# Kernel tuning notes

Hardware: AMD Instinct MI355X
Metric: run time of the kernel (lower is better)

The kernel has to match this reference:

```python
import jax, jax.numpy as jnp
import numpy as np

D_IN = 1024
D_OUT = 1024
NUM_HEADS = 16
HEAD_DIM = D_OUT // NUM_HEADS


def setup_inputs() -> dict:
    key = jax.random.key(0)
    ks = jax.random.split(key, 6)
    s = 0.02
    return {
        "x": jax.random.normal(ks[0], (4, 2048, D_IN), dtype=jnp.float32),
        "Wq": jax.random.normal(ks[1], (D_IN, D_OUT), dtype=jnp.float32) * s,
        "Wk": jax.random.normal(ks[2], (D_IN, D_OUT), dtype=jnp.float32) * s,
        "Wv": jax.random.normal(ks[3], (D_IN, D_OUT), dtype=jnp.float32) * s,
        "Wo": jax.random.normal(ks[4], (D_OUT, D_OUT), dtype=jnp.float32) * s,
        "bo": jax.random.normal(ks[5], (D_OUT,), dtype=jnp.float32) * s,
    }


def reference(x, Wq, Wk, Wv, Wo, bo):
    B, S, _ = x.shape
    # QKV projections (no bias), split into heads: [B, H, S, Dh]
    def split_heads(t):
        return t.reshape(B, S, NUM_HEADS, HEAD_DIM).transpose(0, 2, 1, 3)

    q = split_heads(x @ Wq)
    k = split_heads(x @ Wk)
    v = split_heads(x @ Wv)

    # causal scores [B, H, S, S]; note: original masks BEFORE scaling,
    # but -inf is scale-invariant so softmax(scores/sqrt(d)) with mask is identical.
    scores = jnp.einsum("bhqd,bhkd->bhqk", q, k) / jnp.sqrt(jnp.asarray(HEAD_DIM, x.dtype))
    causal = jnp.tril(jnp.ones((S, S), dtype=bool))
    scores = jnp.where(causal, scores, -jnp.inf)
    attn = jax.nn.softmax(scores, axis=-1)
    # dropout p=0.0 -> identity
    ctx = jnp.einsum("bhqk,bhkd->bhqd", attn, v)  # [B, H, S, Dh]
    ctx = ctx.transpose(0, 2, 1, 3).reshape(B, S, D_OUT)
    return ctx @ Wo + bo
```

## Files before the change

### kernel.cpp

```cpp
#include <hip/hip_runtime.h>
#include <hip/hip_bf16.h>
#include <math.h>


typedef __attribute__((ext_vector_type(8))) short short8;
typedef __attribute__((ext_vector_type(4))) float f32x4;

#define MFMA_BF16(a, b, c) __builtin_amdgcn_mfma_f32_16x16x32_bf16((a), (b), (c), 0, 0, 0)

__device__ __forceinline__ void gld_lds16(const void* g, void* l) {
  __builtin_amdgcn_global_load_lds((const __attribute__((address_space(1))) void*)g,
                                   (__attribute__((address_space(3))) void*)l, 16, 0, 0);
}

__global__ void cast_f32_bf16(const float* __restrict__ in, __hip_bfloat16* __restrict__ out) {
  int i = blockIdx.x * blockDim.x + threadIdx.x;
  float4 v = ((const float4*)in)[i];
  __align__(8) __hip_bfloat16 tmp[4] = {__float2bfloat16(v.x), __float2bfloat16(v.y),
                                        __float2bfloat16(v.z), __float2bfloat16(v.w)};
  ((ushort4*)out)[i] = *(const ushort4*)tmp;
}

__global__ void transpose_cast_w4(const float* __restrict__ W0, const float* __restrict__ W1,
                                  const float* __restrict__ W2, const float* __restrict__ W3,
                                  __hip_bfloat16* __restrict__ T0, __hip_bfloat16* __restrict__ T1,
                                  __hip_bfloat16* __restrict__ T2, __hip_bfloat16* __restrict__ T3) {
  const int z = blockIdx.z;
  const float* W = (z == 0) ? W0 : (z == 1) ? W1 : (z == 2) ? W2 : W3;
  __hip_bfloat16* Wt = (z == 0) ? T0 : (z == 1) ? T1 : (z == 2) ? T2 : T3;
  __shared__ float tile[32][33];
  int tx = threadIdx.x, ty = threadIdx.y;
  int n0 = blockIdx.x * 32, k0 = blockIdx.y * 32;
#pragma unroll
  for (int i = 0; i < 4; ++i)
    tile[ty + i * 8][tx] = W[(size_t)(k0 + ty + i * 8) * 1024 + n0 + tx];
  __syncthreads();
#pragma unroll
  for (int i = 0; i < 4; ++i)
    Wt[(size_t)(n0 + ty + i * 8) * 1024 + k0 + tx] = __float2bfloat16(tile[tx][ty + i * 8]);
}

__global__ __launch_bounds__(256, 2) void gemm_qkv(
    const __hip_bfloat16* __restrict__ A, const __hip_bfloat16* __restrict__ Bt,
    __hip_bfloat16* __restrict__ q, __hip_bfloat16* __restrict__ k,
    __hip_bfloat16* __restrict__ vT) {
  __shared__ __align__(16) __hip_bfloat16 As[128 * 32];
  __shared__ __align__(16) __hip_bfloat16 Bs[128 * 32];
  const int tid = threadIdx.x;
  const int lane = tid & 63, wid = tid >> 6;
  const int quad = lane >> 4, l16 = lane & 15;
  const int part = blockIdx.x >> 3;
  const int n0 = (blockIdx.x & 7) * 128;
  const int gn0 = part * 1024 + n0;
  const int m0 = blockIdx.y * 128;
  const int wm = (wid & 1) * 64, wn = (wid >> 1) * 64;

  f32x4 acc[4][4] = {};

  for (int k0 = 0; k0 < 1024; k0 += 32) {
    __syncthreads();
#pragma unroll
    for (int i = 0; i < 2; ++i) {
      int sbase = __builtin_amdgcn_readfirstlane(wid * 64 + i * 256);
      int s = sbase + lane;
      int row = s >> 2, ch = s & 3;
      gld_lds16(A + (size_t)(m0 + row) * 1024 + k0 + ch * 8, &As[sbase * 8]);
      gld_lds16(Bt + (size_t)(gn0 + row) * 1024 + k0 + ch * 8, &Bs[sbase * 8]);
    }
    __syncthreads();

    short8 af[4], bfr[4];
#pragma unroll
    for (int t = 0; t < 4; ++t) {
      af[t] = *(const short8*)&As[(wm + t * 16 + l16) * 32 + quad * 8];
      bfr[t] = *(const short8*)&Bs[(wn + t * 16 + l16) * 32 + quad * 8];
    }
#pragma unroll
    for (int mt = 0; mt < 4; ++mt)
#pragma unroll
      for (int nt = 0; nt < 4; ++nt)
        acc[mt][nt] = MFMA_BF16(af[mt], bfr[nt], acc[mt][nt]);
  }

  if (part < 2) {
    __hip_bfloat16* C = (part == 0) ? q : k;
#pragma unroll
    for (int mt = 0; mt < 4; ++mt)
#pragma unroll
      for (int nt = 0; nt < 4; ++nt) {
        int row = m0 + wm + mt * 16 + quad * 4;
        int col = n0 + wn + nt * 16 + l16;
#pragma unroll
        for (int r = 0; r < 4; ++r)
          C[(size_t)(row + r) * 1024 + col] = __float2bfloat16(acc[mt][nt][r]);
      }
  } else {
#pragma unroll
    for (int mt = 0; mt < 4; ++mt)
#pragma unroll
      for (int nt = 0; nt < 4; ++nt) {
        int row = m0 + wm + mt * 16 + quad * 4;
        int nn = n0 + wn + nt * 16 + l16;
        __align__(8) __hip_bfloat16 p4[4];
#pragma unroll
        for (int r = 0; r < 4; ++r) p4[r] = __float2bfloat16(acc[mt][nt][r]);
        *(ushort4*)(vT + (size_t)nn * 8192 + row) = *(const ushort4*)p4;
      }
  }
}

__global__ __launch_bounds__(256, 2) void gemm_bt_f32out(
    const __hip_bfloat16* __restrict__ A, const __hip_bfloat16* __restrict__ Bt,
    float* __restrict__ C, const float* __restrict__ bias, int M, int N, int K) {
  __shared__ __align__(16) __hip_bfloat16 As[128 * 32];
  __shared__ __align__(16) __hip_bfloat16 Bs[128 * 32];
  const int tid = threadIdx.x;
  const int lane = tid & 63, wid = tid >> 6;
  const int quad = lane >> 4, l16 = lane & 15;
  const int m0 = blockIdx.y * 128, n0 = blockIdx.x * 128;
  const int wm = (wid & 1) * 64, wn = (wid >> 1) * 64;

  f32x4 acc[4][4] = {};

  for (int k0 = 0; k0 < K; k0 += 32) {
    __syncthreads();
#pragma unroll
    for (int i = 0; i < 2; ++i) {
      int sbase = __builtin_amdgcn_readfirstlane(wid * 64 + i * 256);
      int s = sbase + lane;
      int row = s >> 2, ch = s & 3;
      gld_lds16(A + (size_t)(m0 + row) * K + k0 + ch * 8, &As[sbase * 8]);
      gld_lds16(Bt + (size_t)(n0 + row) * K + k0 + ch * 8, &Bs[sbase * 8]);
    }
    __syncthreads();

    short8 af[4], bfr[4];
#pragma unroll
    for (int t = 0; t < 4; ++t) {
      af[t] = *(const short8*)&As[(wm + t * 16 + l16) * 32 + quad * 8];
      bfr[t] = *(const short8*)&Bs[(wn + t * 16 + l16) * 32 + quad * 8];
    }
#pragma unroll
    for (int mt = 0; mt < 4; ++mt)
#pragma unroll
      for (int nt = 0; nt < 4; ++nt)
        acc[mt][nt] = MFMA_BF16(af[mt], bfr[nt], acc[mt][nt]);
  }

#pragma unroll
  for (int mt = 0; mt < 4; ++mt)
#pragma unroll
    for (int nt = 0; nt < 4; ++nt) {
      int row = m0 + wm + mt * 16 + quad * 4;
      int col = n0 + wn + nt * 16 + l16;
      float b = bias[col];
#pragma unroll
      for (int r = 0; r < 4; ++r)
        C[(size_t)(row + r) * N + col] = acc[mt][nt][r] + b;
    }
}

__global__ __launch_bounds__(256, 2) void attn_kernel(
    const __hip_bfloat16* __restrict__ Q, const __hip_bfloat16* __restrict__ Km,
    const __hip_bfloat16* __restrict__ vT, __hip_bfloat16* __restrict__ ctx) {
  const int bid = blockIdx.x;
  const int p = bid & 7, h = (bid >> 3) & 15, b = bid >> 7;
  const size_t rbase = (size_t)b * 2048;
  const int tid = threadIdx.x, lane = tid & 63, wid = tid >> 6;
  const int quad = lane >> 4, l16 = lane & 15;

  __shared__ __align__(16) __hip_bfloat16 Ks[64 * 72];
  __shared__ __align__(16) __hip_bfloat16 Vs[64 * 72];
  __shared__ __align__(16) __hip_bfloat16 Ps[4][32 * 76];

  const float CSCL = 0.18033688011112042f;
  const float NEG_BIG = -1e30f;

#pragma unroll 1
  for (int sub = 0; sub < 2; ++sub) {
    const int qt = sub ? (15 - p) : p;
    const int q0 = qt * 128;

    short8 qf[2][2];
#pragma unroll
    for (int mt = 0; mt < 2; ++mt)
#pragma unroll
      for (int kc = 0; kc < 2; ++kc)
        qf[mt][kc] = *(const short8*)(Q + (rbase + q0 + wid * 32 + mt * 16 + l16) * 1024 +
                                      h * 64 + kc * 32 + quad * 8);

    f32x4 o[2][4] = {};
    f32x4 lp[2] = {};
    const int wave_max_row = q0 + wid * 32 + 31;
    const int ktiles = q0 / 64 + 2;

#pragma unroll 1
    for (int kt = 0; kt < ktiles; ++kt) {
      const int kbase = kt * 64;
      __syncthreads();
      {
#pragma unroll
        for (int i = 0; i < 2; ++i) {
          int s = tid + i * 256;
          int krow = s >> 3, ch = s & 7;
          *(short8*)&Ks[krow * 72 + ch * 8] =
              *(const short8*)(Km + (rbase + kbase + krow) * 1024 + h * 64 + ch * 8);
        }
      }
      {
#pragma unroll
        for (int i = 0; i < 2; ++i) {
          int s = tid + i * 256;
          int d = s >> 3, ch = s & 7;
          *(short8*)&Vs[d * 72 + ch * 8] =
              *(const short8*)(vT + (size_t)(h * 64 + d) * 8192 + rbase + kbase + ch * 8);
        }
      }
      __syncthreads();

      if (kbase <= wave_max_row) {
        short8 kf[4][2];
#pragma unroll
        for (int nt = 0; nt < 4; ++nt)
#pragma unroll
          for (int kc = 0; kc < 2; ++kc)
            kf[nt][kc] = *(const short8*)&Ks[(nt * 16 + l16) * 72 + kc * 32 + quad * 8];
        f32x4 s[2][4];
#pragma unroll
        for (int mt = 0; mt < 2; ++mt)
#pragma unroll
          for (int nt = 0; nt < 4; ++nt) {
            f32x4 sv = {0.f, 0.f, 0.f, 0.f};
            sv = MFMA_BF16(qf[mt][0], kf[nt][0], sv);
            sv = MFMA_BF16(qf[mt][1], kf[nt][1], sv);
            s[mt][nt] = sv;
          }
        if (kbase + 63 > q0 + wid * 32) {
#pragma unroll
          for (int mt = 0; mt < 2; ++mt)
#pragma unroll
            for (int nt = 0; nt < 4; ++nt)
#pragma unroll
              for (int r = 0; r < 4; ++r) {
                int row = q0 + wid * 32 + mt * 16 + quad * 4 + r;
                int col = kbase + nt * 16 + l16;
                if (col > row) s[mt][nt][r] = NEG_BIG;
              }
        }
#pragma unroll
        for (int mt = 0; mt < 2; ++mt) {
#pragma unroll
          for (int nt = 0; nt < 4; ++nt)
#pragma unroll
            for (int r = 0; r < 4; ++r) {
              float pv = __builtin_amdgcn_exp2f(s[mt][nt][r] * CSCL);
              s[mt][nt][r] = pv;
              lp[mt][r] += pv;
            }
#pragma unroll
          for (int nt = 0; nt < 4; ++nt)
#pragma unroll
            for (int r = 0; r < 4; ++r)
              Ps[wid][(mt * 16 + quad * 4 + r) * 76 + nt * 16 + l16] =
                  __float2bfloat16(s[mt][nt][r]);
        }
        short8 pa[2][2], vf[4][2];
#pragma unroll
        for (int mt = 0; mt < 2; ++mt)
#pragma unroll
          for (int ch = 0; ch < 2; ++ch)
            pa[mt][ch] = *(const short8*)&Ps[wid][(mt * 16 + l16) * 76 + ch * 32 + quad * 8];
#pragma unroll
        for (int dt = 0; dt < 4; ++dt)
#pragma unroll
          for (int ch = 0; ch < 2; ++ch)
            vf[dt][ch] = *(const short8*)&Vs[(dt * 16 + l16) * 72 + ch * 32 + quad * 8];
#pragma unroll
        for (int mt = 0; mt < 2; ++mt)
#pragma unroll
          for (int dt = 0; dt < 4; ++dt) {
            o[mt][dt] = MFMA_BF16(pa[mt][0], vf[dt][0], o[mt][dt]);
            o[mt][dt] = MFMA_BF16(pa[mt][1], vf[dt][1], o[mt][dt]);
          }
      }
    }

#pragma unroll
    for (int mt = 0; mt < 2; ++mt) {
#pragma unroll
      for (int msk = 1; msk <= 8; msk <<= 1)
#pragma unroll
        for (int r = 0; r < 4; ++r)
          lp[mt][r] += __shfl_xor(lp[mt][r], msk, 64);
      float inv[4];
#pragma unroll
      for (int r = 0; r < 4; ++r) inv[r] = 1.f / lp[mt][r];
#pragma unroll
      for (int dt = 0; dt < 4; ++dt)
#pragma unroll
        for (int r = 0; r < 4; ++r)
          ctx[(rbase + q0 + wid * 32 + mt * 16 + quad * 4 + r) * 1024 + h * 64 + dt * 16 + l16] =
              __float2bfloat16(o[mt][dt][r] * inv[r]);
    }
  }
}

extern "C" void kernel_launch(void* const* d_in, const int* in_sizes, int n_in,
                              void* d_out, int out_size, void* d_ws, size_t ws_size,
                              hipStream_t stream) {
  const float* x  = (const float*)d_in[0];
  const float* Wq = (const float*)d_in[1];
  const float* Wk = (const float*)d_in[2];
  const float* Wv = (const float*)d_in[3];
  const float* Wo = (const float*)d_in[4];
  const float* bo = (const float*)d_in[5];
  float* out = (float*)d_out;

  char* ws = (char*)d_ws;
  const size_t MB = 1024ull * 1024ull;
  __hip_bfloat16* q   = (__hip_bfloat16*)(ws);
  __hip_bfloat16* k   = (__hip_bfloat16*)(ws + 16 * MB);
  __hip_bfloat16* vT  = (__hip_bfloat16*)(ws + 32 * MB);
  __hip_bfloat16* woT = (__hip_bfloat16*)(ws + 48 * MB);
  __hip_bfloat16* ctx = q;

  char* outc = (char*)d_out;
  __hip_bfloat16* xb    = (__hip_bfloat16*)(outc);
  __hip_bfloat16* wcatT = (__hip_bfloat16*)(outc + 16 * MB);

  cast_f32_bf16<<<8192, 256, 0, stream>>>(x, xb);
  transpose_cast_w4<<<dim3(32, 32, 4), dim3(32, 8), 0, stream>>>(
      Wq, Wk, Wv, Wo, wcatT, wcatT + 1024 * 1024, wcatT + 2048 * 1024, woT);

  gemm_qkv<<<dim3(24, 64), 256, 0, stream>>>(xb, wcatT, q, k, vT);

  attn_kernel<<<512, 256, 0, stream>>>(q, k, vT, ctx);

  gemm_bt_f32out<<<dim3(8, 64), 256, 0, stream>>>(ctx, woT, out, bo, 8192, 1024, 1024);
}
```

Before: 265.7 us.

## Load K/V fragments directly from global per wave, drop LDS staging and barriers

The attention kernel no longer stages K and V tiles through shared memory with block-wide barriers. Each wave now loads its MFMA fragments straight from global memory and runs only as many key tiles as its own causal extent needs. The softmax scale is folded into the Q projection epilogue, which removes a multiply per score. The cost is that the four waves in a block each re-read K/V from global or L2 instead of sharing one LDS copy, and the loads are not pipelined, so latency may be exposed.

Result: slower. 321.2 us (+20.9%).

```diff
diff --git a/kernel.cpp b/kernel.cpp
--- a/kernel.cpp
+++ b/kernel.cpp
@@ -82,8 +82,10 @@
         acc[mt][nt] = MFMA_BF16(af[mt], bfr[nt], acc[mt][nt]);
   }
 
+  const float CSCL = 0.18033688011112042f;
   if (part < 2) {
     __hip_bfloat16* C = (part == 0) ? q : k;
+    const float scl = (part == 0) ? CSCL : 1.0f;
 #pragma unroll
     for (int mt = 0; mt < 4; ++mt)
 #pragma unroll
@@ -92,7 +94,7 @@
         int col = n0 + wn + nt * 16 + l16;
 #pragma unroll
         for (int r = 0; r < 4; ++r)
-          C[(size_t)(row + r) * 1024 + col] = __float2bfloat16(acc[mt][nt][r]);
+          C[(size_t)(row + r) * 1024 + col] = __float2bfloat16(acc[mt][nt][r] * scl);
       }
   } else {
 #pragma unroll
@@ -169,12 +171,12 @@
   const int tid = threadIdx.x, lane = tid & 63, wid = tid >> 6;
   const int quad = lane >> 4, l16 = lane & 15;
 
-  __shared__ __align__(16) __hip_bfloat16 Ks[64 * 72];
-  __shared__ __align__(16) __hip_bfloat16 Vs[64 * 72];
   __shared__ __align__(16) __hip_bfloat16 Ps[4][32 * 76];
 
-  const float CSCL = 0.18033688011112042f;
   const float NEG_BIG = -1e30f;
+
+  const __hip_bfloat16* Kbase = Km + (rbase + l16) * 1024 + h * 64 + quad * 8;
+  const __hip_bfloat16* Vbase = vT + (size_t)(h * 64 + l16) * 8192 + rbase + quad * 8;
 
 #pragma unroll 1
   for (int sub = 0; sub < 2; ++sub) {
@@ -192,97 +194,77 @@
     f32x4 o[2][4] = {};
     f32x4 lp[2] = {};
     const int wave_max_row = q0 + wid * 32 + 31;
-    const int ktiles = q0 / 64 + 2;
+    const int ktiles_w = (wave_max_row >> 6) + 1;
 
 #pragma unroll 1
-    for (int kt = 0; kt < ktiles; ++kt) {
+    for (int kt = 0; kt < ktiles_w; ++kt) {
       const int kbase = kt * 64;
-      __syncthreads();
-      {
-#pragma unroll
-        for (int i = 0; i < 2; ++i) {
-          int s = tid + i * 256;
-          int krow = s >> 3, ch = s & 7;
-          *(short8*)&Ks[krow * 72 + ch * 8] =
-              *(const short8*)(Km + (rbase + kbase + krow) * 1024 + h * 64 + ch * 8);
+
+      short8 kf[4][2];
+#pragma unroll
+      for (int nt = 0; nt < 4; ++nt)
+#pragma unroll
+        for (int kc = 0; kc < 2; ++kc)
+          kf[nt][kc] = *(const short8*)(Kbase + (size_t)(kbase + nt * 16) * 1024 + kc * 32);
+      short8 vf[4][2];
+#pragma unroll
+      for (int dt = 0; dt < 4; ++dt)
+#pragma unroll
+        for (int ch = 0; ch < 2; ++ch)
+          vf[dt][ch] = *(const short8*)(Vbase + (size_t)dt * 16 * 8192 + kbase + ch * 32);
+
+      f32x4 s[2][4];
+#pragma unroll
+      for (int mt = 0; mt < 2; ++mt)
+#pragma unroll
+        for (int nt = 0; nt < 4; ++nt) {
+          f32x4 sv = {0.f, 0.f, 0.f, 0.f};
+          sv = MFMA_BF16(qf[mt][0], kf[nt][0], sv);
+          sv = MFMA_BF16(qf[mt][1], kf[nt][1], sv);
+          s[mt][nt] = sv;
         }
+      if (kbase + 63 > q0 + wid * 32) {
+#pragma unroll
+        for (int mt = 0; mt < 2; ++mt)
+#pragma unroll
+          for (int nt = 0; nt < 4; ++nt)
+#pragma unroll
+            for (int r = 0; r < 4; ++r) {
+              int row = q0 + wid * 32 + mt * 16 + quad * 4 + r;
+              int col = kbase + nt * 16 + l16;
+              if (col > row) s[mt][nt][r] = NEG_BIG;
+            }
       }
-      {
-#pragma unroll
-        for (int i = 0; i < 2; ++i) {
-          int s = tid + i * 256;
-          int d = s >> 3, ch = s & 7;
-          *(short8*)&Vs[d * 72 + ch * 8] =
-              *(const short8*)(vT + (size_t)(h * 64 + d) * 8192 + rbase + kbase + ch * 8);
+#pragma unroll
+      for (int mt = 0; mt < 2; ++mt) {
+#pragma unroll
+        for (int nt = 0; nt < 4; ++nt)
+#pragma unroll
+          for (int r = 0; r < 4; ++r) {
+            float pv = __builtin_amdgcn_exp2f(s[mt][nt][r]);
+            s[mt][nt][r] = pv;
+            lp[mt][r] += pv;
+          }
+#pragma unroll
+        for (int nt = 0; nt < 4; ++nt)
+#pragma unroll
+          for (int r = 0; r < 4; ++r)
+            Ps[wid][(mt * 16 + quad * 4 + r) * 76 + nt * 16 + l16] =
+                __float2bfloat16(s[mt][nt][r]);
+      }
+      short8 pa[2][2];
+#pragma unroll
+      for (int mt = 0; mt < 2; ++mt)
+#pragma unroll
+        for (int ch = 0; ch < 2; ++ch)
+          pa[mt][ch] = *(const short8*)&Ps[wid][(mt * 16 + l16) * 76 + ch * 32 + quad * 8];
+#pragma unroll
+      for (int mt = 0; mt < 2; ++mt)
+#pragma unroll
+        for (int dt = 0; dt < 4; ++dt) {
+          o[mt][dt] = MFMA_BF16(pa[mt][0], vf[dt][0], o[mt][dt]);
+          o[mt][dt] = MFMA_BF16(pa[mt][1], vf[dt][1], o[mt][dt]);
         }
-      }
-      __syncthreads();
-
-      if (kbase <= wave_max_row) {
-        short8 kf[4][2];
-#pragma unroll
-        for (int nt = 0; nt < 4; ++nt)
-#pragma unroll
-          for (int kc = 0; kc < 2; ++kc)
-            kf[nt][kc] = *(const short8*)&Ks[(nt * 16 + l16) * 72 + kc * 32 + quad * 8];
-        f32x4 s[2][4];
-#pragma unroll
-        for (int mt = 0; mt < 2; ++mt)
-#pragma unroll
-          for (int nt = 0; nt < 4; ++nt) {
-            f32x4 sv = {0.f, 0.f, 0.f, 0.f};
-            sv = MFMA_BF16(qf[mt][0], kf[nt][0], sv);
-            sv = MFMA_BF16(qf[mt][1], kf[nt][1], sv);
-            s[mt][nt] = sv;
-          }
-        if (kbase + 63 > q0 + wid * 32) {
-#pragma unroll
-          for (int mt = 0; mt < 2; ++mt)
-#pragma unroll
-            for (int nt = 0; nt < 4; ++nt)
-#pragma unroll
-              for (int r = 0; r < 4; ++r) {
-                int row = q0 + wid * 32 + mt * 16 + quad * 4 + r;
-                int col = kbase + nt * 16 + l16;
-                if (col > row) s[mt][nt][r] = NEG_BIG;
-              }
-        }
-#pragma unroll
-        for (int mt = 0; mt < 2; ++mt) {
-#pragma unroll
-          for (int nt = 0; nt < 4; ++nt)
-#pragma unroll
-            for (int r = 0; r < 4; ++r) {
-              float pv = __builtin_amdgcn_exp2f(s[mt][nt][r] * CSCL);
-              s[mt][nt][r] = pv;
-              lp[mt][r] += pv;
-            }
-#pragma unroll
-          for (int nt = 0; nt < 4; ++nt)
-#pragma unroll
-            for (int r = 0; r < 4; ++r)
-              Ps[wid][(mt * 16 + quad * 4 + r) * 76 + nt * 16 + l16] =
-                  __float2bfloat16(s[mt][nt][r]);
-        }
-        short8 pa[2][2], vf[4][2];
-#pragma unroll
-        for (int mt = 0; mt < 2; ++mt)
-#pragma unroll
-          for (int ch = 0; ch < 2; ++ch)
-            pa[mt][ch] = *(const short8*)&Ps[wid][(mt * 16 + l16) * 76 + ch * 32 + quad * 8];
-#pragma unroll
-        for (int dt = 0; dt < 4; ++dt)
-#pragma unroll
-          for (int ch = 0; ch < 2; ++ch)
-            vf[dt][ch] = *(const short8*)&Vs[(dt * 16 + l16) * 72 + ch * 32 + quad * 8];
-#pragma unroll
-        for (int mt = 0; mt < 2; ++mt)
-#pragma unroll
-          for (int dt = 0; dt < 4; ++dt) {
-            o[mt][dt] = MFMA_BF16(pa[mt][0], vf[dt][0], o[mt][dt]);
-            o[mt][dt] = MFMA_BF16(pa[mt][1], vf[dt][1], o[mt][dt]);
-          }
-      }
     }
 
 #pragma unroll
```
